# Optimization experiments

Hardware: AMD Instinct MI355X
Metric: run time of the kernel (lower is better)

## Reference

```python
import jax, jax.numpy as jnp
import numpy as np

TEMP1 = 4.0  # self.temp1

def l2norm(x, eps=1e-8):
    # matches torch ref: x / (sqrt(sum(x^2)) + eps)
    return x / (jnp.sqrt(jnp.sum(x * x, axis=-1, keepdims=True)) + eps)

def setup_inputs() -> dict:
    key = jax.random.key(0)
    ks = jax.random.split(key, 8)
    B, C, H, W, D, Q = 32, 1024, 16, 16, 1000, 64
    return {
        "img_features_l": jax.random.normal(ks[0], (B, C, H, W), jnp.float32),
        "img_features_f": jax.random.normal(ks[1], (B, C, H, W), jnp.float32),
        "words_emb": jax.random.normal(ks[2], (B, D, Q), jnp.float32),
        "conv_w": jax.random.normal(ks[3], (D, C), jnp.float32) * 0.02,
        "conv_b": jnp.zeros((D,), jnp.float32),
        "sa_wl": jax.random.normal(ks[4], (D, D), jnp.float32) * 0.02,
        "sa_bl": jnp.zeros((D,), jnp.float32),
        "sa_wg": jax.random.normal(ks[5], (D, D), jnp.float32) * 0.02,
        "sa_bg": jnp.zeros((D,), jnp.float32),
        "sa_wc": jax.random.normal(ks[6], (D,), jnp.float32) * 0.05,
        "sa_bc": jnp.zeros((), jnp.float32),
        "cap_w": jax.random.normal(ks[7], (D,), jnp.float32) * 0.05,
        "cap_b": jnp.zeros((), jnp.float32),
    }

def reference(img_features_l, img_features_f, words_emb, conv_w, conv_b,
              sa_wl, sa_bl, sa_wg, sa_bg, sa_wc, sa_bc, cap_w, cap_b):
    B = img_features_f.shape[0]
    Bw = words_emb.shape[0]
    # 1x1 conv (1024 -> 1000), then flatten spatial and concat frontal+lateral
    f = jnp.einsum('oc,bchw->bohw', conv_w, img_features_f) + conv_b[None, :, None, None]
    l = jnp.einsum('oc,bchw->bohw', conv_w, img_features_l) + conv_b[None, :, None, None]
    img = jnp.concatenate([f.reshape(B, f.shape[1], -1),
                           l.reshape(B, l.shape[1], -1)], axis=2)  # [B, D, S]

    # attention_fn, vectorized over the per-word Python loop (axis i)
    # attn[i,b,s,q] = sum_d img[b,d,s] * words[i,d,q]
    logits = jnp.einsum('bds,idq->ibsq', img, words_emb)            # [Bw,B,S,Q]
    a1 = jax.nn.softmax(logits, axis=-1)                            # softmax over queryL
    a2 = jax.nn.softmax(jnp.swapaxes(a1, -1, -2) * TEMP1, axis=-1)  # [Bw,B,Q,S], softmax over sourceL
    # weightedContext (already transposed to [i,b,q,d])
    wctx = jnp.einsum('bds,ibqs->ibqd', img, a2)                    # [Bw,B,Q,D]

    word_t = jnp.swapaxes(words_emb, 1, 2)[:, None]                 # [Bw,1,Q,D]
    sim_loc = l2norm(wctx * word_t)                                 # [Bw,B,Q,D]
    sim_ave = jnp.mean(sim_loc, axis=2)                             # [Bw,B,D]

    # SA module (dropout in eval mode => identity)
    l_emb = jnp.tanh(jnp.einsum('ibqd,de->ibqe', sim_loc, sa_wl) + sa_bl)
    g_emb = jnp.tanh(jnp.einsum('ibd,de->ibe', sim_ave, sa_wg) + sa_bg)
    common = l_emb * g_emb[:, :, None, :]                           # [Bw,B,Q,D]
    w = jnp.einsum('ibqd,d->ibq', common, sa_wc) + sa_bc            # [Bw,B,Q]
    w = jax.nn.softmax(w, axis=-1)
    new_global = l2norm(jnp.einsum('ibq,ibqd->ibd', w, sim_loc))    # [Bw,B,D]
    sim = jax.nn.sigmoid(jnp.einsum('ibd,d->ib', new_global, cap_w) + cap_b)

    similarities_cap = sim.T                                        # [B, Bw]
    att_maps = a2[jnp.arange(Bw), jnp.arange(Bw)]                   # [Bw,Q,S] (attn[i] per word i)
    return similarities_cap, att_maps
```

## Files before the change

kernel.cpp:

```cpp
#include <hip/hip_runtime.h>
#include <cstdint>

typedef unsigned short u16;
typedef unsigned int   u32;
typedef __attribute__((ext_vector_type(8))) short bf16x8;
typedef __attribute__((ext_vector_type(4))) float f32x4;

#define D_DIM 1000
#define C_IN  1024
#define HW    256
#define S_DIM 512
#define Q_DIM 64

__device__ __forceinline__ u16 f2b(float x) {
    u32 u = __builtin_bit_cast(u32, x);
    u32 r = (u + 0x7FFFu + ((u >> 16) & 1u)) >> 16;
    return (u16)r;
}
__device__ __forceinline__ float b2f(u16 h) {
    u32 u = ((u32)h) << 16;
    return __builtin_bit_cast(float, u);
}
__device__ __forceinline__ float ftanh(float x) {
    float e = __expf(2.f * x);
    return 1.f - 2.f / (e + 1.f);
}

#define GLOAD(ldsptr, gptr) \
    __builtin_amdgcn_global_load_lds( \
        (const __attribute__((address_space(1))) unsigned int*)(gptr), \
        (__attribute__((address_space(3))) unsigned int*)(ldsptr), 16, 0, 0)

__global__ __launch_bounds__(256) void k_prepf(
    const float* __restrict__ feat_l, const float* __restrict__ feat_f,
    u16* __restrict__ fT_hi, u16* __restrict__ fT_lo)
{
    int bid = blockIdx.x;
    int ct = bid & 15, ht = (bid >> 4) & 3, half_ = (bid >> 6) & 1, b = bid >> 7;
    const float* src = (half_ ? feat_l : feat_f) + (size_t)b * C_IN * HW;
    __shared__ float T[64][65];
    int tid = threadIdx.x;
    {
        int cl = tid >> 2, h16 = (tid & 3) * 16;
        const float* p = src + (size_t)(ct * 64 + cl) * 256 + ht * 64 + h16;
        #pragma unroll
        for (int j = 0; j < 4; j++) {
            float4 v = *(const float4*)(p + j * 4);
            T[h16 + j * 4 + 0][cl] = v.x;
            T[h16 + j * 4 + 1][cl] = v.y;
            T[h16 + j * 4 + 2][cl] = v.z;
            T[h16 + j * 4 + 3][cl] = v.w;
        }
    }
    __syncthreads();
    {
        int hl = tid >> 2, c16 = (tid & 3) * 16;
        int srow = b * 512 + half_ * 256 + ht * 64 + hl;
        bf16x8 vh[2], vl[2];
        #pragma unroll
        for (int g = 0; g < 2; g++)
            #pragma unroll
            for (int j = 0; j < 8; j++) {
                float x = T[hl][c16 + g * 8 + j];
                u16 hh = f2b(x);
                vh[g][j] = (short)hh;
                vl[g][j] = (short)f2b(x - b2f(hh));
            }
        size_t o = (size_t)srow * 1024 + ct * 64 + c16;
        *(bf16x8*)(fT_hi + o) = vh[0];
        *(bf16x8*)(fT_hi + o + 8) = vh[1];
        *(bf16x8*)(fT_lo + o) = vl[0];
        *(bf16x8*)(fT_lo + o + 8) = vl[1];
    }
}

__global__ __launch_bounds__(256) void k_prepcw(
    const float* __restrict__ cw, u16* __restrict__ cwh, u16* __restrict__ cwl)
{
    int d = blockIdx.x;
    int c4 = threadIdx.x * 4;
    ushort4 h = make_ushort4(0, 0, 0, 0), lo = make_ushort4(0, 0, 0, 0);
    if (d < D_DIM) {
        float4 v = *(const float4*)(cw + (size_t)d * 1024 + c4);
        float a[4] = {v.x, v.y, v.z, v.w};
        u16* ph = (u16*)&h; u16* pl = (u16*)&lo;
        #pragma unroll
        for (int j = 0; j < 4; j++) {
            ph[j] = f2b(a[j]);
            pl[j] = f2b(a[j] - b2f(ph[j]));
        }
    }
    *(ushort4*)(cwh + (size_t)d * 1024 + c4) = h;
    *(ushort4*)(cwl + (size_t)d * 1024 + c4) = lo;
}

__global__ __launch_bounds__(256) void k_prepw(
    const float* __restrict__ words, u16* __restrict__ wth, u16* __restrict__ wtl)
{
    int i = blockIdx.x >> 4, dt = blockIdx.x & 15;
    const float* src = words + (size_t)i * D_DIM * Q_DIM;
    __shared__ u16 Th[64][72], Tl[64][72];
    int tid = threadIdx.x;
    #pragma unroll
    for (int rep = 0; rep < 4; rep++) {
        int idx = tid + rep * 256;
        int dl = idx >> 4, q4 = (idx & 15) * 4;
        int d = dt * 64 + dl;
        float4 v = make_float4(0.f, 0.f, 0.f, 0.f);
        if (d < D_DIM) v = *(const float4*)(src + (size_t)d * Q_DIM + q4);
        float a[4] = {v.x, v.y, v.z, v.w};
        #pragma unroll
        for (int jj = 0; jj < 4; jj++) {
            u16 hh = f2b(a[jj]);
            Th[dl][q4 + jj] = hh;
            Tl[dl][q4 + jj] = f2b(a[jj] - b2f(hh));
        }
    }
    __syncthreads();
    #pragma unroll
    for (int rep = 0; rep < 2; rep++) {
        int idx = tid + rep * 256;
        int q = idx >> 3, c8 = idx & 7;
        bf16x8 vh, vl;
        #pragma unroll
        for (int jj = 0; jj < 8; jj++) { vh[jj] = (short)Th[c8 * 8 + jj][q]; vl[jj] = (short)Tl[c8 * 8 + jj][q]; }
        size_t doff = (size_t)i * 65536 + (size_t)q * 1024 + dt * 64 + c8 * 8;
        *(bf16x8*)(wth + doff) = vh;
        *(bf16x8*)(wtl + doff) = vl;
    }
}

__global__ __launch_bounds__(256) void k_prep(const float* __restrict__ wl, u16* __restrict__ wlT)
{
    __shared__ float t[64][65];
    int bd = blockIdx.x & 15, be = blockIdx.x >> 4;
    int tx = threadIdx.x & 15, ty = threadIdx.x >> 4;
    #pragma unroll
    for (int rr = 0; rr < 4; rr++) {
        int r = ty * 4 + rr;
        int d = bd * 64 + r;
        int e4 = be * 64 + tx * 4;
        float v0 = 0.f, v1 = 0.f, v2 = 0.f, v3 = 0.f;
        if (d < D_DIM) {
            if (e4 + 3 < D_DIM) {
                float4 v = *reinterpret_cast<const float4*>(wl + (size_t)d * D_DIM + e4);
                v0 = v.x; v1 = v.y; v2 = v.z; v3 = v.w;
            } else {
                if (e4 + 0 < D_DIM) v0 = wl[(size_t)d * D_DIM + e4 + 0];
                if (e4 + 1 < D_DIM) v1 = wl[(size_t)d * D_DIM + e4 + 1];
                if (e4 + 2 < D_DIM) v2 = wl[(size_t)d * D_DIM + e4 + 2];
                if (e4 + 3 < D_DIM) v3 = wl[(size_t)d * D_DIM + e4 + 3];
            }
        }
        t[r][tx * 4 + 0] = v0; t[r][tx * 4 + 1] = v1;
        t[r][tx * 4 + 2] = v2; t[r][tx * 4 + 3] = v3;
    }
    __syncthreads();
    #pragma unroll
    for (int rr = 0; rr < 4; rr++) {
        int r2 = ty * 4 + rr;
        int e = be * 64 + r2;
        int d0 = bd * 64 + tx * 4;
        ushort4 h;
        h.x = f2b(t[tx * 4 + 0][r2]); h.y = f2b(t[tx * 4 + 1][r2]);
        h.z = f2b(t[tx * 4 + 2][r2]); h.w = f2b(t[tx * 4 + 3][r2]);
        *reinterpret_cast<ushort4*>(wlT + (size_t)e * 1024 + d0) = h;
    }
}

__global__ __launch_bounds__(512) void k_convG(
    const u16* __restrict__ fT_hi, const u16* __restrict__ fT_lo,
    const u16* __restrict__ cwh, const u16* __restrict__ cwl,
    const float* __restrict__ cb,
    u16* __restrict__ img_hi, u16* __restrict__ img_lo)
{
    const int bid = blockIdx.x;
    const int mblk = bid >> 2, nt = bid & 3;
    const int m0 = mblk * 256, n0 = nt * 256;

    __shared__ char Ah[16384] __attribute__((aligned(16)));
    __shared__ char Alo[16384] __attribute__((aligned(16)));
    __shared__ char Bh[16384] __attribute__((aligned(16)));
    __shared__ char Blo[16384] __attribute__((aligned(16)));
    __shared__ float cbS[256];

    const int tid = threadIdx.x;
    const int wid = tid >> 6, lane = tid & 63;
    const int wr = wid >> 2, wc = wid & 3;
    const int l15 = lane & 15, l4 = lane >> 4;
    const int sw = (l15 >> 1) & 3;

    if (tid < 256) {
        int d = n0 + tid;
        cbS[tid] = (d < D_DIM) ? cb[d] : 0.f;
    }

    f32x4 acc[8][4] = {};

    for (int k0 = 0; k0 < 1024; k0 += 32) {
        __syncthreads();
        #pragma unroll
        for (int rep = 0; rep < 2; rep++) {
            int idx = tid + rep * 512;
            int row = idx >> 2, slot = idx & 3;
            int kb = (slot ^ ((row >> 1) & 3)) * 16;
            size_t ao = (size_t)(m0 + row) * 2048 + (size_t)k0 * 2 + kb;
            size_t bo = (size_t)(n0 + row) * 2048 + (size_t)k0 * 2 + kb;
            GLOAD(Ah + idx * 16, (const char*)fT_hi + ao);
            GLOAD(Alo + idx * 16, (const char*)fT_lo + ao);
            GLOAD(Bh + idx * 16, (const char*)cwh + bo);
            GLOAD(Blo + idx * 16, (const char*)cwl + bo);
        }
        __syncthreads();
        bf16x8 ah[8], bh[4];
        #pragma unroll
        for (int mf = 0; mf < 8; mf++)
            ah[mf] = *(const bf16x8*)(Ah + (wr * 128 + mf * 16 + l15) * 64 + ((l4 ^ sw) * 16));
        #pragma unroll
        for (int nf = 0; nf < 4; nf++)
            bh[nf] = *(const bf16x8*)(Bh + (wc * 64 + nf * 16 + l15) * 64 + ((l4 ^ sw) * 16));
        #pragma unroll
        for (int mf = 0; mf < 8; mf++)
            #pragma unroll
            for (int nf = 0; nf < 4; nf++)
                acc[mf][nf] = __builtin_amdgcn_mfma_f32_16x16x32_bf16(ah[mf], bh[nf], acc[mf][nf], 0, 0, 0);
        #pragma unroll
        for (int mf = 0; mf < 8; mf++) {
            bf16x8 al = *(const bf16x8*)(Alo + (wr * 128 + mf * 16 + l15) * 64 + ((l4 ^ sw) * 16));
            #pragma unroll
            for (int nf = 0; nf < 4; nf++)
                acc[mf][nf] = __builtin_amdgcn_mfma_f32_16x16x32_bf16(al, bh[nf], acc[mf][nf], 0, 0, 0);
        }
        #pragma unroll
        for (int nf = 0; nf < 4; nf++) {
            bf16x8 bl = *(const bf16x8*)(Blo + (wc * 64 + nf * 16 + l15) * 64 + ((l4 ^ sw) * 16));
            #pragma unroll
            for (int mf = 0; mf < 8; mf++)
                acc[mf][nf] = __builtin_amdgcn_mfma_f32_16x16x32_bf16(ah[mf], bl, acc[mf][nf], 0, 0, 0);
        }
    }
    const int b = m0 >> 9;
    const int sbase = m0 & 511;
    #pragma unroll
    for (int mf = 0; mf < 8; mf++) {
        int srow = sbase + wr * 128 + mf * 16 + l4 * 4;
        #pragma unroll
        for (int nf = 0; nf < 4; nf++) {
            int dcol = n0 + wc * 64 + nf * 16 + l15;
            float bias = cbS[wc * 64 + nf * 16 + l15];
            ushort4 h4, lo4;
            u16* ph = (u16*)&h4; u16* pl = (u16*)&lo4;
            #pragma unroll
            for (int r = 0; r < 4; r++) {
                float v = acc[mf][nf][r] + bias;
                u16 hh = f2b(v);
                ph[r] = hh;
                pl[r] = f2b(v - b2f(hh));
            }
            size_t off = ((size_t)b * 1024 + dcol) * 512 + srow;
            *(ushort4*)(img_hi + off) = h4;
            *(ushort4*)(img_lo + off) = lo4;
        }
    }
}

__global__ __launch_bounds__(256) void k_trans(
    const u16* __restrict__ ih, const u16* __restrict__ il,
    u16* __restrict__ oth, u16* __restrict__ otl)
{
    int bid = blockIdx.x;
    int st = bid & 7, dt = (bid >> 3) & 15, b = bid >> 7;
    const u16* srcH = ih + (size_t)b * 1024 * 512;
    const u16* srcL = il + (size_t)b * 1024 * 512;
    u16* dstH = oth + (size_t)b * 512 * 1024;
    u16* dstL = otl + (size_t)b * 512 * 1024;
    __shared__ u16 Th[64][72], Tl[64][72];
    int tid = threadIdx.x;
    #pragma unroll
    for (int rep = 0; rep < 2; rep++) {
        int idx = tid + rep * 256;
        int dl = idx >> 3, c8 = idx & 7;
        size_t so = (size_t)(dt * 64 + dl) * 512 + st * 64 + c8 * 8;
        bf16x8 vh = *(const bf16x8*)(srcH + so);
        bf16x8 vl = *(const bf16x8*)(srcL + so);
        #pragma unroll
        for (int jj = 0; jj < 8; jj++) { Th[c8 * 8 + jj][dl] = (u16)vh[jj]; Tl[c8 * 8 + jj][dl] = (u16)vl[jj]; }
    }
    __syncthreads();
    #pragma unroll
    for (int rep = 0; rep < 2; rep++) {
        int idx = tid + rep * 256;
        int sl = idx >> 3, c8 = idx & 7;
        bf16x8 vh = *(const bf16x8*)(&Th[sl][c8 * 8]);
        bf16x8 vl = *(const bf16x8*)(&Tl[sl][c8 * 8]);
        size_t doff = (size_t)(st * 64 + sl) * 1024 + dt * 64 + c8 * 8;
        *(bf16x8*)(dstH + doff) = vh;
        *(bf16x8*)(dstL + doff) = vl;
    }
}

__global__ __launch_bounds__(512) void k_logits(
    const u16* __restrict__ wTh, const u16* __restrict__ wTl,
    const u16* __restrict__ iTh, const u16* __restrict__ iTl,
    u16* __restrict__ U, float* __restrict__ Zp, float* __restrict__ out)
{
    const int bid = blockIdx.x;
    const int b = bid >> 4, mt = (bid >> 1) & 7, nt = bid & 1;
    const int m0 = mt * 256, n0 = nt * 256;

    __shared__ char Ah[16384] __attribute__((aligned(16)));
    __shared__ char Alo[16384] __attribute__((aligned(16)));
    __shared__ char Bh[16384] __attribute__((aligned(16)));
    __shared__ char Blo[16384] __attribute__((aligned(16)));

    const int tid = threadIdx.x;
    const int wid = tid >> 6, lane = tid & 63;
    const int wr = wid >> 2, wc = wid & 3;
    const int l15 = lane & 15, l4 = lane >> 4;
    const int sw = (l15 >> 1) & 3;

    f32x4 acc[8][4] = {};

    for (int k0 = 0; k0 < 1024; k0 += 32) {
        __syncthreads();
        #pragma unroll
        for (int rep = 0; rep < 2; rep++) {
            int idx = tid + rep * 512;
            int row = idx >> 2, slot = idx & 3;
            int kb = (slot ^ ((row >> 1) & 3)) * 16;
            size_t ao = (size_t)(m0 + row) * 2048 + (size_t)k0 * 2 + kb;
            size_t bo = ((size_t)b * 512 + n0 + row) * 2048 + (size_t)k0 * 2 + kb;
            GLOAD(Ah + idx * 16, (const char*)wTh + ao);
            GLOAD(Alo + idx * 16, (const char*)wTl + ao);
            GLOAD(Bh + idx * 16, (const char*)iTh + bo);
            GLOAD(Blo + idx * 16, (const char*)iTl + bo);
        }
        __syncthreads();
        bf16x8 ah[8], bh[4];
        #pragma unroll
        for (int mf = 0; mf < 8; mf++)
            ah[mf] = *(const bf16x8*)(Ah + (wr * 128 + mf * 16 + l15) * 64 + ((l4 ^ sw) * 16));
        #pragma unroll
        for (int nf = 0; nf < 4; nf++)
            bh[nf] = *(const bf16x8*)(Bh + (wc * 64 + nf * 16 + l15) * 64 + ((l4 ^ sw) * 16));
        #pragma unroll
        for (int mf = 0; mf < 8; mf++)
            #pragma unroll
            for (int nf = 0; nf < 4; nf++)
                acc[mf][nf] = __builtin_amdgcn_mfma_f32_16x16x32_bf16(ah[mf], bh[nf], acc[mf][nf], 0, 0, 0);
        #pragma unroll
        for (int mf = 0; mf < 8; mf++) {
            bf16x8 al = *(const bf16x8*)(Alo + (wr * 128 + mf * 16 + l15) * 64 + ((l4 ^ sw) * 16));
            #pragma unroll
            for (int nf = 0; nf < 4; nf++)
                acc[mf][nf] = __builtin_amdgcn_mfma_f32_16x16x32_bf16(al, bh[nf], acc[mf][nf], 0, 0, 0);
        }
        #pragma unroll
        for (int nf = 0; nf < 4; nf++) {
            bf16x8 bl = *(const bf16x8*)(Blo + (wc * 64 + nf * 16 + l15) * 64 + ((l4 ^ sw) * 16));
            #pragma unroll
            for (int mf = 0; mf < 8; mf++)
                acc[mf][nf] = __builtin_amdgcn_mfma_f32_16x16x32_bf16(ah[mf], bl, acc[mf][nf], 0, 0, 0);
        }
    }

    float zacc[8][4] = {};
    #pragma unroll
    for (int il = 0; il < 2; il++) {
        int i_glob = mt * 4 + wr * 2 + il;
        bool diag = (i_glob == b);
        #pragma unroll
        for (int nf = 0; nf < 4; nf++) {
            int scol = n0 + wc * 64 + nf * 16 + l15;
            float m = -3.4e38f;
            #pragma unroll
            for (int mm = 0; mm < 4; mm++)
                #pragma unroll
                for (int r = 0; r < 4; r++)
                    m = fmaxf(m, acc[il * 4 + mm][nf][r]);
            m = fmaxf(m, __shfl_xor(m, 16));
            m = fmaxf(m, __shfl_xor(m, 32));
            float e[16], sum = 0.f;
            #pragma unroll
            for (int mm = 0; mm < 4; mm++)
                #pragma unroll
                for (int r = 0; r < 4; r++) {
                    float ev = __expf(acc[il * 4 + mm][nf][r] - m);
                    e[mm * 4 + r] = ev; sum += ev;
                }
            sum += __shfl_xor(sum, 16);
            sum += __shfl_xor(sum, 32);
            float inv = 1.f / sum;
            #pragma unroll
            for (int mm = 0; mm < 4; mm++)
                #pragma unroll
                for (int r = 0; r < 4; r++) {
                    float u = __expf(4.f * e[mm * 4 + r] * inv);
                    u16 ub = f2b(u);
                    zacc[il * 4 + mm][r] += b2f(ub);
                    int iqrow = m0 + wr * 128 + (il * 4 + mm) * 16 + l4 * 4 + r;
                    U[((size_t)b * 2048 + iqrow) * 512 + scol] = ub;
                    if (diag) {
                        int q = iqrow & 63;
                        out[1024 + ((size_t)i_glob * 64 + q) * 512 + scol] = u;
                    }
                }
        }
    }
    #pragma unroll
    for (int mf = 0; mf < 8; mf++)
        #pragma unroll
        for (int r = 0; r < 4; r++) {
            float z = zacc[mf][r];
            z += __shfl_xor(z, 1); z += __shfl_xor(z, 2);
            z += __shfl_xor(z, 4); z += __shfl_xor(z, 8);
            if (l15 == 0) {
                int iqrow = m0 + wr * 128 + mf * 16 + l4 * 4 + r;
                Zp[((size_t)b * 2048 + iqrow) * 8 + nt * 4 + wc] = z;
            }
        }
}

__global__ __launch_bounds__(256) void k_zred(const float* __restrict__ Zp, float* __restrict__ invZf)
{
    int gi = blockIdx.x * 256 + threadIdx.x;
    float4 z0 = *(const float4*)(Zp + (size_t)gi * 8);
    float4 z1 = *(const float4*)(Zp + (size_t)gi * 8 + 4);
    invZf[gi] = 1.f / (z0.x + z0.y + z0.z + z0.w + z1.x + z1.y + z1.z + z1.w);
}

__global__ __launch_bounds__(256) void k_attmap2(float* __restrict__ out)
{
    const int i = blockIdx.x;
    float* am = out + 1024 + (size_t)i * Q_DIM * S_DIM;
    int q = threadIdx.x >> 2, ch = threadIdx.x & 3;
    float s = 0.f;
    for (int ss = ch * 128; ss < ch * 128 + 128; ss++) s += am[(size_t)q * S_DIM + ss];
    s += __shfl_xor(s, 1);
    s += __shfl_xor(s, 2);
    float iz = 1.f / s;
    for (int ss = ch * 128; ss < ch * 128 + 128; ss++) am[(size_t)q * S_DIM + ss] *= iz;
}

__global__ __launch_bounds__(512) void k_wctx(
    const u16* __restrict__ img_hi, const u16* __restrict__ U,
    const float* __restrict__ invZf,
    const u16* __restrict__ wTh, const u16* __restrict__ wTl,
    u16* __restrict__ vbuf, float* __restrict__ ssqp)
{
    const int bid = blockIdx.x;
    const int b = bid >> 5, mt = (bid >> 3) & 3, nt = bid & 7;
    const int m0 = mt * 256, n0 = nt * 256;

    __shared__ char At[32768] __attribute__((aligned(16)));
    __shared__ char Bt[32768] __attribute__((aligned(16)));
    __shared__ float izS[256];

    const int tid = threadIdx.x;
    const int wid = tid >> 6, lane = tid & 63;
    const int wr = wid >> 2, wc = wid & 3;
    const int l15 = lane & 15, l4 = lane >> 4;
    const int sw = l15 & 7;

    if (tid < 256) izS[tid] = invZf[b * 2048 + n0 + tid];

    f32x4 acc[8][4] = {};

    for (int k0 = 0; k0 < 512; k0 += 64) {
        __syncthreads();
        #pragma unroll
        for (int rep = 0; rep < 4; rep++) {
            int idx = tid + rep * 512;
            int row = idx >> 3, slot = idx & 7;
            int kb = (slot ^ (row & 7)) * 16;
            GLOAD(At + idx * 16, (const char*)img_hi + ((size_t)b * 1024 + m0 + row) * 1024 + (size_t)k0 * 2 + kb);
            GLOAD(Bt + idx * 16, (const char*)U + ((size_t)b * 2048 + n0 + row) * 1024 + (size_t)k0 * 2 + kb);
        }
        __syncthreads();
        #pragma unroll
        for (int kf = 0; kf < 2; kf++) {
            bf16x8 a[8], bb[4];
            #pragma unroll
            for (int mf = 0; mf < 8; mf++)
                a[mf] = *(const bf16x8*)(At + (wr * 128 + mf * 16 + l15) * 128 + (((kf * 4 + l4) ^ sw) * 16));
            #pragma unroll
            for (int nf = 0; nf < 4; nf++)
                bb[nf] = *(const bf16x8*)(Bt + (wc * 64 + nf * 16 + l15) * 128 + (((kf * 4 + l4) ^ sw) * 16));
            #pragma unroll
            for (int mf = 0; mf < 8; mf++)
                #pragma unroll
                for (int nf = 0; nf < 4; nf++)
                    acc[mf][nf] = __builtin_amdgcn_mfma_f32_16x16x32_bf16(a[mf], bb[nf], acc[mf][nf], 0, 0, 0);
        }
    }

    #pragma unroll
    for (int nf = 0; nf < 4; nf++) {
        int col = wc * 64 + nf * 16 + l15;
        int iq = n0 + col;
        float iz = izS[col];
        size_t wtoff = (size_t)iq * 1024;
        float s_nf = 0.f;
        #pragma unroll
        for (int mf = 0; mf < 8; mf++) {
            int d0 = m0 + wr * 128 + mf * 16 + l4 * 4;
            ushort4 wh = *(const ushort4*)(wTh + wtoff + d0);
            ushort4 wl = *(const ushort4*)(wTl + wtoff + d0);
            const u16* pwh = (const u16*)&wh;
            const u16* pwl = (const u16*)&wl;
            ushort4 vo;
            u16* pv = (u16*)&vo;
            #pragma unroll
            for (int r = 0; r < 4; r++) {
                float wv = b2f(pwh[r]) + b2f(pwl[r]);
                float v = acc[mf][nf][r] * iz * wv;
                s_nf = fmaf(v, v, s_nf);
                pv[r] = f2b(v);
            }
            *(ushort4*)(vbuf + ((size_t)b * 2048 + iq) * 1024 + d0) = vo;
        }
        s_nf += __shfl_xor(s_nf, 16);
        s_nf += __shfl_xor(s_nf, 32);
        if (l4 == 0) ssqp[((size_t)b * 2048 + iq) * 4 + mt] = s_nf;
    }
}

__global__ __launch_bounds__(256) void k_post(
    const u16* __restrict__ vbuf, const float* __restrict__ ssqp,
    float* __restrict__ invn_ws, u16* __restrict__ simave_bf)
{
    const int pair = blockIdx.x;
    __shared__ float invnS[64];
    const int tid = threadIdx.x;
    if (tid < 64) {
        size_t o = ((size_t)pair * 64 + tid) * 4;
        float s = ssqp[o] + ssqp[o + 1] + ssqp[o + 2] + ssqp[o + 3];
        float n = 1.f / (sqrtf(s) + 1e-8f);
        invnS[tid] = n;
        invn_ws[pair * 64 + tid] = n;
    }
    __syncthreads();
    int d0 = tid * 4;
    ushort4 o4 = make_ushort4(0, 0, 0, 0);
    if (d0 < D_DIM) {
        float a0 = 0.f, a1 = 0.f, a2 = 0.f, a3 = 0.f;
        const u16* vb = vbuf + (size_t)pair * 65536;
        for (int q = 0; q < 64; q++) {
            float n = invnS[q];
            ushort4 v = *(const ushort4*)(vb + q * 1024 + d0);
            a0 = fmaf(b2f(v.x), n, a0); a1 = fmaf(b2f(v.y), n, a1);
            a2 = fmaf(b2f(v.z), n, a2); a3 = fmaf(b2f(v.w), n, a3);
        }
        o4.x = f2b(a0 * (1.f / 64.f)); o4.y = f2b(a1 * (1.f / 64.f));
        o4.z = f2b(a2 * (1.f / 64.f)); o4.w = f2b(a3 * (1.f / 64.f));
    }
    *(ushort4*)(simave_bf + (size_t)pair * 1024 + d0) = o4;
}

__global__ __launch_bounds__(512) void k_g2M(
    const u16* __restrict__ simave_bf, const u16* __restrict__ wgT,
    const float* __restrict__ bg, const float* __restrict__ wc,
    float* __restrict__ g2)
{
    const int mt = blockIdx.x >> 2, nt = blockIdx.x & 3;
    const int m0 = mt * 256, n0 = nt * 256;

    __shared__ char Al[32768] __attribute__((aligned(16)));
    __shared__ char Bl[32768] __attribute__((aligned(16)));
    __shared__ float bgS[256], wcS[256];

    const int tid = threadIdx.x;
    const int wid = tid >> 6, lane = tid & 63;
    const int wr = wid >> 2, wc_ = wid & 3;
    const int l15 = lane & 15, l4 = lane >> 4;
    const int sw = l15 & 7;

    if (tid < 256) {
        int e = n0 + tid;
        bgS[tid] = (e < D_DIM) ? bg[e] : 0.f;
        wcS[tid] = (e < D_DIM) ? wc[e] : 0.f;
    }

    f32x4 acc[8][4] = {};

    for (int k0 = 0; k0 < 1024; k0 += 64) {
        __syncthreads();
        #pragma unroll
        for (int rep = 0; rep < 4; rep++) {
            int idx = tid + rep * 512;
            int row = idx >> 3, slot = idx & 7;
            int kb = (slot ^ (row & 7)) * 16;
            GLOAD(Al + idx * 16, (const char*)simave_bf + (size_t)(m0 + row) * 2048 + (size_t)k0 * 2 + kb);
            GLOAD(Bl + idx * 16, (const char*)wgT + (size_t)(n0 + row) * 2048 + (size_t)k0 * 2 + kb);
        }
        __syncthreads();
        #pragma unroll
        for (int kf = 0; kf < 2; kf++) {
            bf16x8 a[8], bb[4];
            #pragma unroll
            for (int mf = 0; mf < 8; mf++)
                a[mf] = *(const bf16x8*)(Al + (wr * 128 + mf * 16 + l15) * 128 + (((kf * 4 + l4) ^ sw) * 16));
            #pragma unroll
            for (int nf = 0; nf < 4; nf++)
                bb[nf] = *(const bf16x8*)(Bl + (wc_ * 64 + nf * 16 + l15) * 128 + (((kf * 4 + l4) ^ sw) * 16));
            #pragma unroll
            for (int mf = 0; mf < 8; mf++)
                #pragma unroll
                for (int nf = 0; nf < 4; nf++)
                    acc[mf][nf] = __builtin_amdgcn_mfma_f32_16x16x32_bf16(a[mf], bb[nf], acc[mf][nf], 0, 0, 0);
        }
    }

    #pragma unroll
    for (int mf = 0; mf < 8; mf++) {
        int p = m0 + wr * 128 + mf * 16 + l4 * 4;
        #pragma unroll
        for (int nf = 0; nf < 4; nf++) {
            int cl = wc_ * 64 + nf * 16 + l15;
            float bgv = bgS[cl], wcv = wcS[cl];
            #pragma unroll
            for (int r = 0; r < 4; r++)
                g2[(size_t)(p + r) * 1024 + n0 + cl] = ftanh(acc[mf][nf][r] + bgv) * wcv;
        }
    }
}

__global__ __launch_bounds__(512) void k_saG(
    const u16* __restrict__ vbuf, const u16* __restrict__ wlT,
    const float* __restrict__ invn_ws, const float* __restrict__ g2_ws,
    const float* __restrict__ bl, float* __restrict__ wspart)
{
    const int bid = blockIdx.x;
    const int wg = (bid & 7) * 128 + (bid >> 3);
    const int mt = wg >> 2, nt = wg & 3;
    const int m0 = mt * 256, n0 = nt * 256;

    __shared__ char Al[32768] __attribute__((aligned(16)));
    __shared__ char Bl[32768] __attribute__((aligned(16)));
    __shared__ float invnS[256];
    __shared__ float blS[256];
    __shared__ float g2S[4 * 256];

    const int tid = threadIdx.x;
    const int wid = tid >> 6, lane = tid & 63;
    const int wr = wid >> 2, wc = wid & 3;
    const int l15 = lane & 15, l4 = lane >> 4;
    const int sw = l15 & 7;

    if (tid < 256) {
        invnS[tid] = invn_ws[m0 + tid];
        int e = n0 + tid;
        blS[tid] = (e < D_DIM) ? bl[e] : 0.f;
    }
    #pragma unroll
    for (int rep = 0; rep < 2; rep++) {
        int idx = tid + rep * 512;
        int p = idx >> 8, el = idx & 255;
        g2S[idx] = g2_ws[(size_t)((m0 >> 6) + p) * 1024 + n0 + el];
    }

    f32x4 acc[8][4] = {};

    for (int k0 = 0; k0 < 1024; k0 += 64) {
        __syncthreads();
        #pragma unroll
        for (int rep = 0; rep < 4; rep++) {
            int idx = tid + rep * 512;
            int row = idx >> 3, slot = idx & 7;
            int kb = (slot ^ (row & 7)) * 16;
            GLOAD(Al + idx * 16, (const char*)vbuf + (size_t)(m0 + row) * 2048 + (size_t)k0 * 2 + kb);
            GLOAD(Bl + idx * 16, (const char*)wlT + (size_t)(n0 + row) * 2048 + (size_t)k0 * 2 + kb);
        }
        __syncthreads();
        #pragma unroll
        for (int kf = 0; kf < 2; kf++) {
            bf16x8 a[8], bb[4];
            #pragma unroll
            for (int mf = 0; mf < 8; mf++)
                a[mf] = *(const bf16x8*)(Al + (wr * 128 + mf * 16 + l15) * 128 + (((kf * 4 + l4) ^ sw) * 16));
            #pragma unroll
            for (int nf = 0; nf < 4; nf++)
                bb[nf] = *(const bf16x8*)(Bl + (wc * 64 + nf * 16 + l15) * 128 + (((kf * 4 + l4) ^ sw) * 16));
            #pragma unroll
            for (int mf = 0; mf < 8; mf++)
                #pragma unroll
                for (int nf = 0; nf < 4; nf++)
                    acc[mf][nf] = __builtin_amdgcn_mfma_f32_16x16x32_bf16(a[mf], bb[nf], acc[mf][nf], 0, 0, 0);
        }
    }

    #pragma unroll
    for (int mf = 0; mf < 8; mf++) {
        int mrow = wr * 128 + mf * 16 + l4 * 4;
        #pragma unroll
        for (int r = 0; r < 4; r++) {
            float inv = invnS[mrow + r];
            int p = (mrow + r) >> 6;
            float s = 0.f;
            #pragma unroll
            for (int nf = 0; nf < 4; nf++) {
                int el = wc * 64 + nf * 16 + l15;
                float x = acc[mf][nf][r] * inv + blS[el];
                s += ftanh(x) * g2S[p * 256 + el];
            }
            s += __shfl_xor(s, 1);
            s += __shfl_xor(s, 2);
            s += __shfl_xor(s, 4);
            s += __shfl_xor(s, 8);
            if (l15 == 0)
                wspart[(size_t)(nt * 4 + wc) * 65536 + m0 + mrow + r] = s;
        }
    }
}

__global__ __launch_bounds__(256) void k_sa2(
    const float* __restrict__ wspart, const float* __restrict__ invn_ws,
    const u16* __restrict__ vbuf, const float* __restrict__ capw,
    const float* __restrict__ capb, float* __restrict__ out)
{
    const int pair = blockIdx.x;
    const u16* vb = vbuf + (size_t)pair * 65536;

    __shared__ float wiS[64];
    __shared__ float red[8];

    const int tid = threadIdx.x;

    if (tid < 64) {
        float x = 0.f;
        #pragma unroll
        for (int c = 0; c < 16; c++) x += wspart[(size_t)c * 65536 + pair * 64 + tid];
        float m = x;
        #pragma unroll
        for (int mk = 1; mk < 64; mk <<= 1) m = fmaxf(m, __shfl_xor(m, mk));
        float e = __expf(x - m);
        float Z = e;
        #pragma unroll
        for (int mk = 1; mk < 64; mk <<= 1) Z += __shfl_xor(Z, mk);
        wiS[tid] = (e / Z) * invn_ws[pair * 64 + tid];
    }
    __syncthreads();

    float s1 = 0.f, s2 = 0.f;
    int d0 = tid * 4;
    if (d0 < D_DIM) {
        float a0 = 0.f, a1 = 0.f, a2 = 0.f, a3 = 0.f;
        for (int q = 0; q < 64; q++) {
            float wq = wiS[q];
            ushort4 v = *(const ushort4*)(vb + q * 1024 + d0);
            a0 = fmaf(wq, b2f(v.x), a0); a1 = fmaf(wq, b2f(v.y), a1);
            a2 = fmaf(wq, b2f(v.z), a2); a3 = fmaf(wq, b2f(v.w), a3);
        }
        float4 cw4 = *(const float4*)(capw + d0);
        s1 = a0 * cw4.x + a1 * cw4.y + a2 * cw4.z + a3 * cw4.w;
        s2 = a0 * a0 + a1 * a1 + a2 * a2 + a3 * a3;
    }
    #pragma unroll
    for (int mk = 1; mk < 64; mk <<= 1) { s1 += __shfl_xor(s1, mk); s2 += __shfl_xor(s2, mk); }
    if ((tid & 63) == 0) { red[tid >> 6] = s1; red[4 + (tid >> 6)] = s2; }
    __syncthreads();
    if (tid == 0) {
        float S1 = red[0] + red[1] + red[2] + red[3];
        float S2 = red[4] + red[5] + red[6] + red[7];
        float val = S1 / (sqrtf(S2) + 1e-8f) + capb[0];
        out[pair] = 1.f / (1.f + __expf(-val));
    }
}

extern "C" void kernel_launch(void* const* d_in, const int* in_sizes, int n_in,
                              void* d_out, int out_size, void* d_ws, size_t ws_size,
                              hipStream_t stream)
{
    const float* feat_l = (const float*)d_in[0];
    const float* feat_f = (const float*)d_in[1];
    const float* words  = (const float*)d_in[2];
    const float* conv_w = (const float*)d_in[3];
    const float* conv_b = (const float*)d_in[4];
    const float* sa_wl  = (const float*)d_in[5];
    const float* sa_bl  = (const float*)d_in[6];
    const float* sa_wg  = (const float*)d_in[7];
    const float* sa_bg  = (const float*)d_in[8];
    const float* sa_wc  = (const float*)d_in[9];
    const float* cap_w  = (const float*)d_in[11];
    const float* cap_b  = (const float*)d_in[12];
    float* out = (float*)d_out;

    char* ws = (char*)d_ws;
    u16*   featT_hi  = (u16*)(ws);
    u16*   featT_lo  = (u16*)(ws + 33554432);
    u16*   imgT_hi   = (u16*)(ws + 67108864);
    u16*   imgT_lo   = (u16*)(ws + 100663296);
    u16*   vbuf      = (u16*)(ws);
    u16*   img_hi    = (u16*)(ws + 134217728);
    u16*   wgT       = (u16*)(ws + 134217728);
    u16*   img_lo    = (u16*)(ws + 167772160);
    u16*   U         = (u16*)(ws + 167772160);
    float* wspart    = (float*)(ws + 167772160);
    u16*   wT_hi     = (u16*)(ws + 234881024);
    u16*   simave_bf = (u16*)(ws + 234881024);
    u16*   wT_lo     = (u16*)(ws + 239075328);
    u16*   cw_hi     = (u16*)(ws + 243269632);
    float* Zp        = (float*)(ws + 243269632);
    u16*   cw_lo     = (u16*)(ws + 245366784);
    float* invZf     = (float*)(ws + 245366784);
    float* ssqp      = (float*)(ws + 245628928);
    float* invn      = (float*)(ws + 246677504);
    u16*   wlT       = (u16*)(ws + 247463936);
    float* g2        = (float*)(ws + 249561088);

    hipLaunchKernelGGL(k_prepf, dim3(4096), dim3(256), 0, stream,
                       feat_l, feat_f, featT_hi, featT_lo);
    hipLaunchKernelGGL(k_prepcw, dim3(1024), dim3(256), 0, stream,
                       conv_w, cw_hi, cw_lo);
    hipLaunchKernelGGL(k_prepw, dim3(512), dim3(256), 0, stream,
                       words, wT_hi, wT_lo);
    hipLaunchKernelGGL(k_prep, dim3(256), dim3(256), 0, stream, sa_wl, wlT);
    hipLaunchKernelGGL(k_convG, dim3(256), dim3(512), 0, stream,
                       featT_hi, featT_lo, cw_hi, cw_lo, conv_b, img_hi, img_lo);
    hipLaunchKernelGGL(k_trans, dim3(4096), dim3(256), 0, stream,
                       img_hi, img_lo, imgT_hi, imgT_lo);
    hipLaunchKernelGGL(k_logits, dim3(512), dim3(512), 0, stream,
                       wT_hi, wT_lo, imgT_hi, imgT_lo, U, Zp, out);
    hipLaunchKernelGGL(k_zred, dim3(256), dim3(256), 0, stream, Zp, invZf);
    hipLaunchKernelGGL(k_attmap2, dim3(32), dim3(256), 0, stream, out);
    hipLaunchKernelGGL(k_wctx, dim3(1024), dim3(512), 0, stream,
                       img_hi, U, invZf, wT_hi, wT_lo, vbuf, ssqp);
    hipLaunchKernelGGL(k_prep, dim3(256), dim3(256), 0, stream, sa_wg, wgT);
    hipLaunchKernelGGL(k_post, dim3(1024), dim3(256), 0, stream,
                       vbuf, ssqp, invn, simave_bf);
    hipLaunchKernelGGL(k_g2M, dim3(16), dim3(512), 0, stream,
                       simave_bf, wgT, sa_bg, sa_wc, g2);
    hipLaunchKernelGGL(k_saG, dim3(1024), dim3(512), 0, stream,
                       vbuf, wlT, invn, g2, sa_bl, wspart);
    hipLaunchKernelGGL(k_sa2, dim3(1024), dim3(256), 0, stream,
                       wspart, invn, vbuf, cap_w, cap_b, out);
}
```

Before: 835.7 us.

## Double-buffer LDS tiles in all MFMA GEMM kernels to overlap loads with compute

Each of the five GEMM-style kernels (convG, logits, the weighted-context GEMM, the global SA GEMM and saG) now allocates a single 128KB LDS region split into two stages. The next K-slice is issued into the alternate buffer before the MFMA work on the current one. This removes one barrier per iteration and hides global-to-LDS load latency behind matrix math. The cost is double the LDS footprint per block, which could limit how many blocks fit per CU, and it relies on the barrier at the end of each iteration to drain the outstanding asynchronous loads.

```diff
diff --git a/kernel.cpp b/kernel.cpp
--- a/kernel.cpp
+++ b/kernel.cpp
@@ -178,10 +178,7 @@
     const int mblk = bid >> 2, nt = bid & 3;
     const int m0 = mblk * 256, n0 = nt * 256;
 
-    __shared__ char Ah[16384] __attribute__((aligned(16)));
-    __shared__ char Alo[16384] __attribute__((aligned(16)));
-    __shared__ char Bh[16384] __attribute__((aligned(16)));
-    __shared__ char Blo[16384] __attribute__((aligned(16)));
+    __shared__ char LDS[131072] __attribute__((aligned(16)));
     __shared__ float cbS[256];
 
     const int tid = threadIdx.x;
@@ -195,10 +192,8 @@
         cbS[tid] = (d < D_DIM) ? cb[d] : 0.f;
     }
 
-    f32x4 acc[8][4] = {};
-
-    for (int k0 = 0; k0 < 1024; k0 += 32) {
-        __syncthreads();
+    auto stage = [&](int buf, int k0) {
+        char* base = LDS + buf * 65536;
         #pragma unroll
         for (int rep = 0; rep < 2; rep++) {
             int idx = tid + rep * 512;
@@ -206,12 +201,24 @@
             int kb = (slot ^ ((row >> 1) & 3)) * 16;
             size_t ao = (size_t)(m0 + row) * 2048 + (size_t)k0 * 2 + kb;
             size_t bo = (size_t)(n0 + row) * 2048 + (size_t)k0 * 2 + kb;
-            GLOAD(Ah + idx * 16, (const char*)fT_hi + ao);
-            GLOAD(Alo + idx * 16, (const char*)fT_lo + ao);
-            GLOAD(Bh + idx * 16, (const char*)cwh + bo);
-            GLOAD(Blo + idx * 16, (const char*)cwl + bo);
-        }
-        __syncthreads();
+            GLOAD(base + idx * 16, (const char*)fT_hi + ao);
+            GLOAD(base + 16384 + idx * 16, (const char*)fT_lo + ao);
+            GLOAD(base + 32768 + idx * 16, (const char*)cwh + bo);
+            GLOAD(base + 49152 + idx * 16, (const char*)cwl + bo);
+        }
+    };
+
+    f32x4 acc[8][4] = {};
+
+    stage(0, 0);
+    __syncthreads();
+    int cur = 0;
+    for (int k0 = 0; k0 < 1024; k0 += 32) {
+        if (k0 + 32 < 1024) stage(cur ^ 1, k0 + 32);
+        const char* Ah = LDS + cur * 65536;
+        const char* Alo = Ah + 16384;
+        const char* Bh = Ah + 32768;
+        const char* Blo = Ah + 49152;
         bf16x8 ah[8], bh[4];
         #pragma unroll
         for (int mf = 0; mf < 8; mf++)
@@ -238,6 +245,8 @@
             for (int mf = 0; mf < 8; mf++)
                 acc[mf][nf] = __builtin_amdgcn_mfma_f32_16x16x32_bf16(ah[mf], bl, acc[mf][nf], 0, 0, 0);
         }
+        __syncthreads();
+        cur ^= 1;
     }
     const int b = m0 >> 9;
     const int sbase = m0 & 511;
@@ -308,10 +317,7 @@
     const int b = bid >> 4, mt = (bid >> 1) & 7, nt = bid & 1;
     const int m0 = mt * 256, n0 = nt * 256;
 
-    __shared__ char Ah[16384] __attribute__((aligned(16)));
-    __shared__ char Alo[16384] __attribute__((aligned(16)));
-    __shared__ char Bh[16384] __attribute__((aligned(16)));
-    __shared__ char Blo[16384] __attribute__((aligned(16)));
+    __shared__ char LDS[131072] __attribute__((aligned(16)));
 
     const int tid = threadIdx.x;
     const int wid = tid >> 6, lane = tid & 63;
@@ -319,10 +325,8 @@
     const int l15 = lane & 15, l4 = lane >> 4;
     const int sw = (l15 >> 1) & 3;
 
-    f32x4 acc[8][4] = {};
-
-    for (int k0 = 0; k0 < 1024; k0 += 32) {
-        __syncthreads();
+    auto stage = [&](int buf, int k0) {
+        char* base = LDS + buf * 65536;
         #pragma unroll
         for (int rep = 0; rep < 2; rep++) {
             int idx = tid + rep * 512;
@@ -330,12 +334,24 @@
             int kb = (slot ^ ((row >> 1) & 3)) * 16;
             size_t ao = (size_t)(m0 + row) * 2048 + (size_t)k0 * 2 + kb;
             size_t bo = ((size_t)b * 512 + n0 + row) * 2048 + (size_t)k0 * 2 + kb;
-            GLOAD(Ah + idx * 16, (const char*)wTh + ao);
-            GLOAD(Alo + idx * 16, (const char*)wTl + ao);
-            GLOAD(Bh + idx * 16, (const char*)iTh + bo);
-            GLOAD(Blo + idx * 16, (const char*)iTl + bo);
-        }
-        __syncthreads();
+            GLOAD(base + idx * 16, (const char*)wTh + ao);
+            GLOAD(base + 16384 + idx * 16, (const char*)wTl + ao);
+            GLOAD(base + 32768 + idx * 16, (const char*)iTh + bo);
+            GLOAD(base + 49152 + idx * 16, (const char*)iTl + bo);
+        }
+    };
+
+    f32x4 acc[8][4] = {};
+
+    stage(0, 0);
+    __syncthreads();
+    int cur = 0;
+    for (int k0 = 0; k0 < 1024; k0 += 32) {
+        if (k0 + 32 < 1024) stage(cur ^ 1, k0 + 32);
+        const char* Ah = LDS + cur * 65536;
+        const char* Alo = Ah + 16384;
+        const char* Bh = Ah + 32768;
+        const char* Blo = Ah + 49152;
         bf16x8 ah[8], bh[4];
         #pragma unroll
         for (int mf = 0; mf < 8; mf++)
@@ -362,6 +378,8 @@
             for (int mf = 0; mf < 8; mf++)
                 acc[mf][nf] = __builtin_amdgcn_mfma_f32_16x16x32_bf16(ah[mf], bl, acc[mf][nf], 0, 0, 0);
         }
+        __syncthreads();
+        cur ^= 1;
     }
 
     float zacc[8][4] = {};
@@ -452,8 +470,7 @@
     const int b = bid >> 5, mt = (bid >> 3) & 3, nt = bid & 7;
     const int m0 = mt * 256, n0 = nt * 256;
 
-    __shared__ char At[32768] __attribute__((aligned(16)));
-    __shared__ char Bt[32768] __attribute__((aligned(16)));
+    __shared__ char LDS[131072] __attribute__((aligned(16)));
     __shared__ float izS[256];
 
     const int tid = threadIdx.x;
@@ -464,19 +481,27 @@
 
     if (tid < 256) izS[tid] = invZf[b * 2048 + n0 + tid];
 
-    f32x4 acc[8][4] = {};
-
-    for (int k0 = 0; k0 < 512; k0 += 64) {
-        __syncthreads();
+    auto stage = [&](int buf, int k0) {
+        char* base = LDS + buf * 65536;
         #pragma unroll
         for (int rep = 0; rep < 4; rep++) {
             int idx = tid + rep * 512;
             int row = idx >> 3, slot = idx & 7;
             int kb = (slot ^ (row & 7)) * 16;
-            GLOAD(At + idx * 16, (const char*)img_hi + ((size_t)b * 1024 + m0 + row) * 1024 + (size_t)k0 * 2 + kb);
-            GLOAD(Bt + idx * 16, (const char*)U + ((size_t)b * 2048 + n0 + row) * 1024 + (size_t)k0 * 2 + kb);
-        }
-        __syncthreads();
+            GLOAD(base + idx * 16, (const char*)img_hi + ((size_t)b * 1024 + m0 + row) * 1024 + (size_t)k0 * 2 + kb);
+            GLOAD(base + 32768 + idx * 16, (const char*)U + ((size_t)b * 2048 + n0 + row) * 1024 + (size_t)k0 * 2 + kb);
+        }
+    };
+
+    f32x4 acc[8][4] = {};
+
+    stage(0, 0);
+    __syncthreads();
+    int cur = 0;
+    for (int k0 = 0; k0 < 512; k0 += 64) {
+        if (k0 + 64 < 512) stage(cur ^ 1, k0 + 64);
+        const char* At = LDS + cur * 65536;
+        const char* Bt = At + 32768;
         #pragma unroll
         for (int kf = 0; kf < 2; kf++) {
             bf16x8 a[8], bb[4];
@@ -492,6 +517,8 @@
                 for (int nf = 0; nf < 4; nf++)
                     acc[mf][nf] = __builtin_amdgcn_mfma_f32_16x16x32_bf16(a[mf], bb[nf], acc[mf][nf], 0, 0, 0);
         }
+        __syncthreads();
+        cur ^= 1;
     }
 
     #pragma unroll
@@ -565,8 +592,7 @@
     const int mt = blockIdx.x >> 2, nt = blockIdx.x & 3;
     const int m0 = mt * 256, n0 = nt * 256;
 
-    __shared__ char Al[32768] __attribute__((aligned(16)));
-    __shared__ char Bl[32768] __attribute__((aligned(16)));
+    __shared__ char LDS[131072] __attribute__((aligned(16)));
     __shared__ float bgS[256], wcS[256];
 
     const int tid = threadIdx.x;
@@ -581,19 +607,27 @@
         wcS[tid] = (e < D_DIM) ? wc[e] : 0.f;
     }
 
-    f32x4 acc[8][4] = {};
-
-    for (int k0 = 0; k0 < 1024; k0 += 64) {
-        __syncthreads();
+    auto stage = [&](int buf, int k0) {
+        char* base = LDS + buf * 65536;
         #pragma unroll
         for (int rep = 0; rep < 4; rep++) {
             int idx = tid + rep * 512;
             int row = idx >> 3, slot = idx & 7;
             int kb = (slot ^ (row & 7)) * 16;
-            GLOAD(Al + idx * 16, (const char*)simave_bf + (size_t)(m0 + row) * 2048 + (size_t)k0 * 2 + kb);
-            GLOAD(Bl + idx * 16, (const char*)wgT + (size_t)(n0 + row) * 2048 + (size_t)k0 * 2 + kb);
-        }
-        __syncthreads();
+            GLOAD(base + idx * 16, (const char*)simave_bf + (size_t)(m0 + row) * 2048 + (size_t)k0 * 2 + kb);
+            GLOAD(base + 32768 + idx * 16, (const char*)wgT + (size_t)(n0 + row) * 2048 + (size_t)k0 * 2 + kb);
+        }
+    };
+
+    f32x4 acc[8][4] = {};
+
+    stage(0, 0);
+    __syncthreads();
+    int cur = 0;
+    for (int k0 = 0; k0 < 1024; k0 += 64) {
+        if (k0 + 64 < 1024) stage(cur ^ 1, k0 + 64);
+        const char* Al = LDS + cur * 65536;
+        const char* Bl = Al + 32768;
         #pragma unroll
         for (int kf = 0; kf < 2; kf++) {
             bf16x8 a[8], bb[4];
@@ -609,6 +643,8 @@
                 for (int nf = 0; nf < 4; nf++)
                     acc[mf][nf] = __builtin_amdgcn_mfma_f32_16x16x32_bf16(a[mf], bb[nf], acc[mf][nf], 0, 0, 0);
         }
+        __syncthreads();
+        cur ^= 1;
     }
 
     #pragma unroll
@@ -635,8 +671,7 @@
     const int mt = wg >> 2, nt = wg & 3;
     const int m0 = mt * 256, n0 = nt * 256;
 
-    __shared__ char Al[32768] __attribute__((aligned(16)));
-    __shared__ char Bl[32768] __attribute__((aligned(16)));
+    __shared__ char LDS[131072] __attribute__((aligned(16)));
     __shared__ float invnS[256];
     __shared__ float blS[256];
     __shared__ float g2S[4 * 256];
@@ -659,19 +694,27 @@
         g2S[idx] = g2_ws[(size_t)((m0 >> 6) + p) * 1024 + n0 + el];
     }
 
-    f32x4 acc[8][4] = {};
-
-    for (int k0 = 0; k0 < 1024; k0 += 64) {
-        __syncthreads();
+    auto stage = [&](int buf, int k0) {
+        char* base = LDS + buf * 65536;
         #pragma unroll
         for (int rep = 0; rep < 4; rep++) {
             int idx = tid + rep * 512;
             int row = idx >> 3, slot = idx & 7;
             int kb = (slot ^ (row & 7)) * 16;
-            GLOAD(Al + idx * 16, (const char*)vbuf + (size_t)(m0 + row) * 2048 + (size_t)k0 * 2 + kb);
-            GLOAD(Bl + idx * 16, (const char*)wlT + (size_t)(n0 + row) * 2048 + (size_t)k0 * 2 + kb);
-        }
-        __syncthreads();
+            GLOAD(base + idx * 16, (const char*)vbuf + (size_t)(m0 + row) * 2048 + (size_t)k0 * 2 + kb);
+            GLOAD(base + 32768 + idx * 16, (const char*)wlT + (size_t)(n0 + row) * 2048 + (size_t)k0 * 2 + kb);
+        }
+    };
+
+    f32x4 acc[8][4] = {};
+
+    stage(0, 0);
+    __syncthreads();
+    int cur = 0;
+    for (int k0 = 0; k0 < 1024; k0 += 64) {
+        if (k0 + 64 < 1024) stage(cur ^ 1, k0 + 64);
+        const char* Al = LDS + cur * 65536;
+        const char* Bl = Al + 32768;
         #pragma unroll
         for (int kf = 0; kf < 2; kf++) {
             bf16x8 a[8], bb[4];
@@ -687,6 +730,8 @@
                 for (int nf = 0; nf < 4; nf++)
                     acc[mf][nf] = __builtin_amdgcn_mfma_f32_16x16x32_bf16(a[mf], bb[nf], acc[mf][nf], 0, 0, 0);
         }
+        __syncthreads();
+        cur ^= 1;
     }
 
     #pragma unroll
```

Measured after the change: 737.6 us. 1.13x faster.
